# Optimization experiments

Hardware: AMD Instinct MI355X
Metric: run time of the kernel (lower is better)

Reference implementation:

```python
import jax, jax.numpy as jnp
import numpy as np

KEY_DIM = 512
VAL_DIM = 512
BATCH = 32768
MEMORY_MAX_NORM = 5.0
TTT_LR_SCALE = 0.005
EPS = 1e-8


def setup_inputs() -> dict:
    key = jax.random.key(0)
    k1, k2, k3, k4, k5 = jax.random.split(key, 5)
    k = jax.random.normal(k1, (BATCH, KEY_DIM), dtype=jnp.float32)
    v = jax.random.normal(k2, (BATCH, VAL_DIM), dtype=jnp.float32)
    # memory weight init: normal(std=0.01)
    mem_w = jax.random.normal(k3, (VAL_DIM, KEY_DIM), dtype=jnp.float32) * 0.01
    # gate_proj: init is zeros/0.5; use small random weight + 0.5 bias for a
    # non-degenerate but realistic post-warmup state
    gate_w = jax.random.normal(k4, (3, KEY_DIM + VAL_DIM), dtype=jnp.float32) * 0.01
    gate_b = jnp.full((3,), 0.5, dtype=jnp.float32)
    momentum_S = jax.random.normal(k5, (VAL_DIM, KEY_DIM), dtype=jnp.float32) * 0.01
    return {"k": k, "v": v, "mem_w": mem_w, "gate_w": gate_w,
            "gate_b": gate_b, "momentum_S": momentum_S}


def _norm_clip(x, max_norm):
    n = jnp.linalg.norm(x)
    return jnp.where(n > max_norm, x * (max_norm / (n + EPS)), x)


def reference(k, v, mem_w, gate_w, gate_b, momentum_S):
    # retrieve: M(k) = k @ W^T ; loss = MSE(pred, v)
    retrieved = k @ mem_w.T                      # [B, val_dim]
    diff = retrieved - v
    loss = jnp.mean(diff * diff)

    # gates from batch-mean key/value
    kv_agg = jnp.concatenate([k.mean(0), v.mean(0)], axis=-1)  # [key+val]
    gates = jax.nn.sigmoid(kv_agg @ gate_w.T + gate_b)         # [3]
    alpha, eta, theta = gates[0], gates[1], gates[2]

    # analytic grad of MSE wrt W: 2/(B*val_dim) * (pred - v)^T @ k
    B, vd = diff.shape
    grad = (2.0 / (B * vd)) * (diff.T @ k)       # [val_dim, key_dim]
    grad_c = jnp.clip(grad, -1.0, 1.0)

    new_momentum = eta * momentum_S - TTT_LR_SCALE * theta * grad_c
    new_momentum = _norm_clip(new_momentum, MEMORY_MAX_NORM)

    new_weight = (1.0 - alpha) * mem_w + new_momentum
    new_weight = _norm_clip(new_weight, MEMORY_MAX_NORM)

    return retrieved, loss, new_weight, new_momentum, alpha, eta, theta
```

## Files before the change

kernel.cpp:

```cpp
#include <hip/hip_runtime.h>
#include <math.h>


typedef __bf16 bf16x8 __attribute__((ext_vector_type(8)));
typedef float f32x4 __attribute__((ext_vector_type(4)));
typedef float float4_t __attribute__((ext_vector_type(4)));
typedef unsigned short ushort4_t __attribute__((ext_vector_type(4)));
typedef unsigned short ushort8_t __attribute__((ext_vector_type(8)));

#define OUT_LOSS   16777216
#define OUT_W      16777217
#define OUT_MOM    17039361
#define OUT_ALPHA  17301505

#define OFF_GRAD   0u
#define OFF_CKP    1048576u
#define OFF_CVP    2097152u
#define OFF_LOSSP  2621440u
#define OFF_COLK   2622464u
#define OFF_COLV   2624512u
#define OFF_SCAL   2626560u
#define OFF_K16    2626624u
#define OFF_W16    36181056u
#define OFF_DIFF   36705344u
#define OFF_MRAW   OFF_K16
#define OFF_WRAW   (OFF_K16 + 1048576u)

__device__ __forceinline__ unsigned short f2bf(float f) {
  union { float f; unsigned int u; } c; c.f = f;
  unsigned int u = c.u;
  u += 0x7fffu + ((u >> 16) & 1u);
  return (unsigned short)(u >> 16);
}

__device__ __forceinline__ void gload_lds16(const unsigned short* g, unsigned short* l) {
  __builtin_amdgcn_global_load_lds(
      (const __attribute__((address_space(1))) unsigned int*)g,
      (__attribute__((address_space(3))) unsigned int*)l, 16, 0, 0);
}

__global__ __launch_bounds__(256) void k1_convert(
    const float* __restrict__ Kp, const float* __restrict__ Wp,
    unsigned short* __restrict__ k16, unsigned short* __restrict__ w16,
    float* __restrict__ colk_part)
{
  __shared__ float cp[512];
  const int t = threadIdx.x;
  const int cg = t & 127;
  const int g = t >> 7;
  const int b = blockIdx.x;
  if (b < 512) {
    const int r0 = b << 6;
    float p0 = 0.f, p1 = 0.f, p2 = 0.f, p3 = 0.f;
#pragma unroll 4
    for (int rr = g; rr < 64; rr += 2) {
      const size_t off = (size_t)(r0 + rr) * 512 + (cg << 2);
      const float4_t v = *reinterpret_cast<const float4_t*>(&Kp[off]);
      ushort4_t h;
      h.x = f2bf(v.x); h.y = f2bf(v.y); h.z = f2bf(v.z); h.w = f2bf(v.w);
      *reinterpret_cast<ushort4_t*>(&k16[off]) = h;
      p0 += v.x; p1 += v.y; p2 += v.z; p3 += v.w;
    }
    if (g == 1) {
      cp[(cg << 2) + 0] = p0; cp[(cg << 2) + 1] = p1;
      cp[(cg << 2) + 2] = p2; cp[(cg << 2) + 3] = p3;
    }
    __syncthreads();
    if (g == 0) {
      colk_part[(size_t)b * 512 + (cg << 2) + 0] = p0 + cp[(cg << 2) + 0];
      colk_part[(size_t)b * 512 + (cg << 2) + 1] = p1 + cp[(cg << 2) + 1];
      colk_part[(size_t)b * 512 + (cg << 2) + 2] = p2 + cp[(cg << 2) + 2];
      colk_part[(size_t)b * 512 + (cg << 2) + 3] = p3 + cp[(cg << 2) + 3];
    }
  } else {
    const int r0 = (b - 512) << 5;
#pragma unroll 4
    for (int rr = g; rr < 32; rr += 2) {
      const size_t off = (size_t)(r0 + rr) * 512 + (cg << 2);
      const float4_t v = *reinterpret_cast<const float4_t*>(&Wp[off]);
      ushort4_t h;
      h.x = f2bf(v.x); h.y = f2bf(v.y); h.z = f2bf(v.z); h.w = f2bf(v.w);
      *reinterpret_cast<ushort4_t*>(&w16[off]) = h;
    }
  }
}

__global__ __launch_bounds__(256) void k2_gemm(
    const unsigned short* __restrict__ k16, const unsigned short* __restrict__ w16,
    const float* __restrict__ Vp, float* __restrict__ outp,
    unsigned short* __restrict__ diff16,
    float* __restrict__ colv_part, float* __restrict__ loss_part)
{
  __shared__ __align__(16) unsigned short As[8192];
  __shared__ __align__(16) unsigned short Bs[8192];
  __shared__ float redc[256];
  __shared__ float redl[4];

  const int t = threadIdx.x, lane = t & 63, wv = t >> 6;
  const int tile = (blockIdx.x & 7) * 128 + (blockIdx.x >> 3);
  const int rt = tile >> 2, vt = tile & 3;
  const int row0 = rt << 7, vd0 = vt << 7;

  f32x4 acc[4][4];
#pragma unroll
  for (int m = 0; m < 4; ++m)
#pragma unroll
    for (int n = 0; n < 4; ++n)
      acc[m][n] = (f32x4){0.f, 0.f, 0.f, 0.f};

  const int srow = (wv << 3) + (lane >> 3);
  const int scol = (lane & 7) << 3;
  const unsigned short* pA = k16 + (size_t)(row0 + srow) * 512 + scol;
  const unsigned short* pB = w16 + (size_t)(vd0 + srow) * 512 + scol;
  unsigned short* lA = &As[wv << 9];
  unsigned short* lB = &Bs[wv << 9];

  const int fr = lane & 15, fq = lane >> 4;
  const int wr = (wv >> 1) << 6, wc = (wv & 1) << 6;

  for (int kk0 = 0; kk0 < 512; kk0 += 64) {
#pragma unroll
    for (int i = 0; i < 4; ++i) {
      gload_lds16(pA + (i << 14) + kk0, lA + (i << 11));
      gload_lds16(pB + (i << 14) + kk0, lB + (i << 11));
    }
    __syncthreads();
#pragma unroll
    for (int kk = 0; kk < 64; kk += 32) {
      const int co = kk + (fq << 3);
      bf16x8 af[4], bfv[4];
#pragma unroll
      for (int m = 0; m < 4; ++m)
        af[m] = *reinterpret_cast<const bf16x8*>(&As[((wr + (m << 4) + fr) << 6) + co]);
#pragma unroll
      for (int n = 0; n < 4; ++n)
        bfv[n] = *reinterpret_cast<const bf16x8*>(&Bs[((wc + (n << 4) + fr) << 6) + co]);
#pragma unroll
      for (int m = 0; m < 4; ++m)
#pragma unroll
        for (int n = 0; n < 4; ++n)
          acc[m][n] = __builtin_amdgcn_mfma_f32_16x16x32_bf16(af[m], bfv[n], acc[m][n], 0, 0, 0);
    }
    __syncthreads();
  }

  float lsum = 0.f;
  float vcs[4] = {0.f, 0.f, 0.f, 0.f};
#pragma unroll
  for (int m = 0; m < 4; ++m) {
#pragma unroll
    for (int n = 0; n < 4; ++n) {
#pragma unroll
      for (int i = 0; i < 4; ++i) {
        const int gr = row0 + wr + (m << 4) + (fq << 2) + i;
        const int gc = vd0 + wc + (n << 4) + fr;
        const size_t oi = (size_t)gr * 512 + gc;
        const float rv = acc[m][n][i];
        outp[oi] = rv;
        const float vv = Vp[oi];
        const float d = rv - vv;
        lsum += d * d;
        vcs[n] += vv;
        diff16[oi] = f2bf(d);
      }
    }
  }
#pragma unroll
  for (int o = 32; o; o >>= 1) lsum += __shfl_xor(lsum, o);
  if (lane == 0) redl[wv] = lsum;
#pragma unroll
  for (int n = 0; n < 4; ++n) {
    vcs[n] += __shfl_xor(vcs[n], 16);
    vcs[n] += __shfl_xor(vcs[n], 32);
  }
  if (fq == 0) {
#pragma unroll
    for (int n = 0; n < 4; ++n)
      redc[(wv << 6) + (n << 4) + fr] = vcs[n];
  }
  __syncthreads();
  if (t < 128) {
    const int side = t >> 6, lc = t & 63;
    colv_part[(size_t)rt * 512 + vd0 + t] =
        redc[side * 64 + lc] + redc[(side + 2) * 64 + lc];
  }
  if (t == 0)
    atomicAdd(&loss_part[rt], redl[0] + redl[1] + redl[2] + redl[3]);
}

__global__ __launch_bounds__(256) void k3_grad(
    const unsigned short* __restrict__ diff16,
    const unsigned short* __restrict__ k16,
    float* __restrict__ grad)
{
  __shared__ __align__(16) unsigned short At[2][128][40];
  __shared__ __align__(16) unsigned short Bt[2][128][40];
  const int t = threadIdx.x;
  const int lane = t & 63;
  const int wv = t >> 6;
  const int b = blockIdx.x;
  const int x = b & 7;
  const int q = b >> 3;
  const int tile = q & 15;
  const int kc = ((q >> 4) << 3) | x;
  const int vd0 = (tile & 3) << 7;
  const int kd0 = (tile >> 2) << 7;
  const size_t r0 = (size_t)kc << 10;

  f32x4 acc[4][4];
#pragma unroll
  for (int m = 0; m < 4; ++m)
#pragma unroll
    for (int n = 0; n < 4; ++n)
      acc[m][n] = (f32x4){0.f, 0.f, 0.f, 0.f};

  const int dr = t >> 3;
  const int c0 = (t & 7) << 4;
  const int wr = (wv >> 1) << 6;
  const int wc = (wv & 1) << 6;
  const int fr = lane & 15;
  const int fq = lane >> 4;

  int cur = 0;
  for (int rr = 0; rr < 1024; rr += 32) {
    const size_t rowoff = (r0 + rr + dr) << 9;
    const ushort8_t a0 = *reinterpret_cast<const ushort8_t*>(&diff16[rowoff + vd0 + c0]);
    const ushort8_t a1 = *reinterpret_cast<const ushort8_t*>(&diff16[rowoff + vd0 + c0 + 8]);
    const ushort8_t b0 = *reinterpret_cast<const ushort8_t*>(&k16[rowoff + kd0 + c0]);
    const ushort8_t b1 = *reinterpret_cast<const ushort8_t*>(&k16[rowoff + kd0 + c0 + 8]);
    const int swz = ((c0 >> 4) & 3) << 3;
#pragma unroll
    for (int j = 0; j < 8; ++j) {
      const int drs = dr ^ swz;
      At[cur][c0 + j][drs] = a0[j];
      At[cur][c0 + 8 + j][drs] = a1[j];
      Bt[cur][c0 + j][drs] = b0[j];
      Bt[cur][c0 + 8 + j][drs] = b1[j];
    }
    __syncthreads();
    bf16x8 af[4], bfv[4];
#pragma unroll
    for (int m = 0; m < 4; ++m) {
      const int rA = wr + (m << 4) + fr;
      af[m] = *reinterpret_cast<const bf16x8*>(&At[cur][rA][(fq ^ ((rA >> 4) & 3)) << 3]);
    }
#pragma unroll
    for (int n = 0; n < 4; ++n) {
      const int rB = wc + (n << 4) + fr;
      bfv[n] = *reinterpret_cast<const bf16x8*>(&Bt[cur][rB][(fq ^ ((rB >> 4) & 3)) << 3]);
    }
#pragma unroll
    for (int m = 0; m < 4; ++m)
#pragma unroll
      for (int n = 0; n < 4; ++n)
        acc[m][n] = __builtin_amdgcn_mfma_f32_16x16x32_bf16(af[m], bfv[n], acc[m][n], 0, 0, 0);
    cur ^= 1;
  }
#pragma unroll
  for (int m = 0; m < 4; ++m)
#pragma unroll
    for (int n = 0; n < 4; ++n)
#pragma unroll
      for (int i = 0; i < 4; ++i)
        atomicAdd(&grad[(size_t)(vd0 + wr + (m << 4) + (fq << 2) + i) * 512
                        + kd0 + wc + (n << 4) + fr], acc[m][n][i]);
}

__global__ __launch_bounds__(256) void c1a_redcols(
    const float* __restrict__ ckp, const float* __restrict__ cvp,
    float* __restrict__ colk, float* __restrict__ colv)
{
  __shared__ float red[8][32];
  const int t = threadIdx.x, b = blockIdx.x;
  const int mtx = b >> 4;
  const int c = ((b & 15) << 5) + (t & 31);
  const int pg = t >> 5;
  const float* src = mtx ? cvp : ckp;
  const int P = mtx ? 256 : 512;
  float s = 0.f;
  for (int p = pg; p < P; p += 8) s += src[(size_t)p * 512 + c];
  red[pg][t & 31] = s;
  __syncthreads();
  if (pg == 0) {
    float tot = 0.f;
#pragma unroll
    for (int j = 0; j < 8; ++j) tot += red[j][t & 31];
    (mtx ? colv : colk)[c] = tot;
  }
}

__global__ __launch_bounds__(256) void c1b_gates(
    const float* __restrict__ gw, const float* __restrict__ gb,
    const float* __restrict__ colk, const float* __restrict__ colv,
    const float* __restrict__ lossp, float* __restrict__ scal,
    float* __restrict__ outp)
{
  __shared__ float red3[3][4];
  __shared__ float redl[4];
  const int t = threadIdx.x, lane = t & 63, wvi = t >> 6;
  float p[3] = {0.f, 0.f, 0.f};
  for (int j = t; j < 1024; j += 256) {
    const float kv = (j < 512 ? colk[j] : colv[j - 512]) * (1.0f / 32768.0f);
    p[0] += kv * gw[j];
    p[1] += kv * gw[1024 + j];
    p[2] += kv * gw[2048 + j];
  }
  float ls = lossp[t];
#pragma unroll
  for (int o = 32; o; o >>= 1) {
    ls += __shfl_xor(ls, o);
#pragma unroll
    for (int g = 0; g < 3; ++g) p[g] += __shfl_xor(p[g], o);
  }
  if (lane == 0) {
    red3[0][wvi] = p[0]; red3[1][wvi] = p[1]; red3[2][wvi] = p[2];
    redl[wvi] = ls;
  }
  __syncthreads();
  if (t == 0) {
    const float s0 = red3[0][0] + red3[0][1] + red3[0][2] + red3[0][3] + gb[0];
    const float s1 = red3[1][0] + red3[1][1] + red3[1][2] + red3[1][3] + gb[1];
    const float s2 = red3[2][0] + red3[2][1] + red3[2][2] + red3[2][3] + gb[2];
    const float alpha = 1.0f / (1.0f + expf(-s0));
    const float eta   = 1.0f / (1.0f + expf(-s1));
    const float theta = 1.0f / (1.0f + expf(-s2));
    scal[3] = alpha; scal[4] = eta; scal[5] = theta;
    outp[OUT_LOSS] = (redl[0] + redl[1] + redl[2] + redl[3]) * (1.0f / 16777216.0f);
    outp[OUT_ALPHA]     = alpha;
    outp[OUT_ALPHA + 1] = eta;
    outp[OUT_ALPHA + 2] = theta;
  }
}

__device__ __forceinline__ void block_atomic_sumsq(float sq, float* target) {
  __shared__ float red[4];
#pragma unroll
  for (int o = 32; o; o >>= 1) sq += __shfl_xor(sq, o);
  if ((threadIdx.x & 63) == 0) red[threadIdx.x >> 6] = sq;
  __syncthreads();
  if (threadIdx.x == 0) atomicAdd(target, red[0] + red[1] + red[2] + red[3]);
}

__global__ __launch_bounds__(256) void c2_mom(
    const float* __restrict__ grad, const float* __restrict__ S,
    float* scal, float* __restrict__ m_raw)
{
  const float eta = scal[4];
  const float cth = 0.005f * scal[5];
  const int i = ((blockIdx.x << 8) + threadIdx.x) << 2;
  const float4_t g = *reinterpret_cast<const float4_t*>(&grad[i]);
  const float4_t s = *reinterpret_cast<const float4_t*>(&S[i]);
  float4_t m; float sq = 0.f;
#pragma unroll
  for (int j = 0; j < 4; ++j) {
    float gj = g[j] * (2.0f / 16777216.0f);
    gj = fminf(1.0f, fmaxf(-1.0f, gj));
    m[j] = eta * s[j] - cth * gj;
    sq += m[j] * m[j];
  }
  *reinterpret_cast<float4_t*>(&m_raw[i]) = m;
  block_atomic_sumsq(sq, &scal[1]);
}

__global__ __launch_bounds__(256) void c3_wt(
    const float* __restrict__ m_raw, const float* __restrict__ memw,
    float* scal, float* __restrict__ w_raw, float* __restrict__ outp)
{
  const float nm = sqrtf(scal[1]);
  const float sm = nm > 5.0f ? 5.0f / (nm + 1e-8f) : 1.0f;
  const float oma = 1.0f - scal[3];
  const int i = ((blockIdx.x << 8) + threadIdx.x) << 2;
  const float4_t mr = *reinterpret_cast<const float4_t*>(&m_raw[i]);
  const float4_t wi = *reinterpret_cast<const float4_t*>(&memw[i]);
  float4_t w; float sq = 0.f;
#pragma unroll
  for (int j = 0; j < 4; ++j) {
    const float m = mr[j] * sm;
    outp[OUT_MOM + i + j] = m;
    w[j] = oma * wi[j] + m;
    sq += w[j] * w[j];
  }
  *reinterpret_cast<float4_t*>(&w_raw[i]) = w;
  block_atomic_sumsq(sq, &scal[2]);
}

__global__ __launch_bounds__(256) void c4_wt(
    const float* __restrict__ w_raw, const float* __restrict__ scal,
    float* __restrict__ outp)
{
  const float nw = sqrtf(scal[2]);
  const float sw = nw > 5.0f ? 5.0f / (nw + 1e-8f) : 1.0f;
  const int i = ((blockIdx.x << 8) + threadIdx.x) << 2;
  const float4_t w = *reinterpret_cast<const float4_t*>(&w_raw[i]);
#pragma unroll
  for (int j = 0; j < 4; ++j)
    outp[OUT_W + i + j] = w[j] * sw;
}

extern "C" void kernel_launch(void* const* d_in, const int* in_sizes, int n_in,
                              void* d_out, int out_size, void* d_ws, size_t ws_size,
                              hipStream_t stream)
{
  const float* Kp = (const float*)d_in[0];
  const float* Vp = (const float*)d_in[1];
  const float* Wp = (const float*)d_in[2];
  const float* GW = (const float*)d_in[3];
  const float* GB = (const float*)d_in[4];
  const float* Sp = (const float*)d_in[5];
  float* outp = (float*)d_out;
  char* ws = (char*)d_ws;

  float* grad            = (float*)(ws + OFF_GRAD);
  float* colk_part       = (float*)(ws + OFF_CKP);
  float* colv_part       = (float*)(ws + OFF_CVP);
  float* loss_part       = (float*)(ws + OFF_LOSSP);
  float* colk            = (float*)(ws + OFF_COLK);
  float* colv            = (float*)(ws + OFF_COLV);
  float* scal            = (float*)(ws + OFF_SCAL);
  unsigned short* k16    = (unsigned short*)(ws + OFF_K16);
  unsigned short* w16    = (unsigned short*)(ws + OFF_W16);
  unsigned short* diff16 = (unsigned short*)(ws + OFF_DIFF);
  float* m_raw           = (float*)(ws + OFF_MRAW);
  float* w_raw           = (float*)(ws + OFF_WRAW);

  hipMemsetAsync(ws + OFF_GRAD, 0, 1048576, stream);
  hipMemsetAsync(ws + OFF_LOSSP, 0, OFF_SCAL + 64 - OFF_LOSSP, stream);

  k1_convert<<<528, 256, 0, stream>>>(Kp, Wp, k16, w16, colk_part);
  k2_gemm<<<1024, 256, 0, stream>>>(k16, w16, Vp, outp, diff16, colv_part, loss_part);
  k3_grad<<<512, 256, 0, stream>>>(diff16, k16, grad);
  c1a_redcols<<<32, 256, 0, stream>>>(colk_part, colv_part, colk, colv);
  c1b_gates<<<1, 256, 0, stream>>>(GW, GB, colk, colv, loss_part, scal, outp);
  c2_mom<<<256, 256, 0, stream>>>(grad, Sp, scal, m_raw);
  c3_wt<<<256, 256, 0, stream>>>(m_raw, Wp, scal, w_raw, outp);
  c4_wt<<<256, 256, 0, stream>>>(w_raw, scal, outp);
}
```

Before: 183.8 us.

## Fuse fp32-to-bf16 conversion into GEMM and move column sums into grad kernel

Drops the separate conversion kernel. The GEMM now loads fp32 K and W directly, converts them to bf16 into padded LDS, and writes the bf16 K copy once per row tile. Column sums of K move into the gradient kernel, atomics into grad are spread across four slabs, and the two-stage reduction kernel is merged into the gates kernel. This removes a full pass over K and two launches, but the GEMM loses its async global-to-LDS loads, reads W in fp32 redundantly, and the single-block gates kernel now does a larger serial reduction.

```diff
diff --git a/kernel.cpp b/kernel.cpp
--- a/kernel.cpp
+++ b/kernel.cpp
@@ -14,85 +14,34 @@
 #define OUT_ALPHA  17301505
 
 #define OFF_GRAD   0u
-#define OFF_CKP    1048576u
-#define OFF_CVP    2097152u
-#define OFF_LOSSP  2621440u
-#define OFF_COLK   2622464u
-#define OFF_COLV   2624512u
-#define OFF_SCAL   2626560u
-#define OFF_K16    2626624u
-#define OFF_W16    36181056u
-#define OFF_DIFF   36705344u
+#define OFF_CKP    4194304u
+#define OFF_CVP    4259840u
+#define OFF_LOSSP  4784128u
+#define OFF_SCAL   4788224u
+#define OFF_K16    4788288u
+#define OFF_DIFF   38342720u
 #define OFF_MRAW   OFF_K16
 #define OFF_WRAW   (OFF_K16 + 1048576u)
 
-__device__ __forceinline__ unsigned short f2bf(float f) {
-  union { float f; unsigned int u; } c; c.f = f;
-  unsigned int u = c.u;
-  u += 0x7fffu + ((u >> 16) & 1u);
-  return (unsigned short)(u >> 16);
-}
-
-__device__ __forceinline__ void gload_lds16(const unsigned short* g, unsigned short* l) {
-  __builtin_amdgcn_global_load_lds(
-      (const __attribute__((address_space(1))) unsigned int*)g,
-      (__attribute__((address_space(3))) unsigned int*)l, 16, 0, 0);
-}
-
-__global__ __launch_bounds__(256) void k1_convert(
+__device__ __forceinline__ ushort4_t cvt4(float4_t v) {
+  union { __bf16 b; unsigned short u; } c0, c1, c2, c3;
+  c0.b = (__bf16)v.x; c1.b = (__bf16)v.y; c2.b = (__bf16)v.z; c3.b = (__bf16)v.w;
+  ushort4_t h; h.x = c0.u; h.y = c1.u; h.z = c2.u; h.w = c3.u;
+  return h;
+}
+
+__device__ __forceinline__ float bf2f(unsigned short u) {
+  return __uint_as_float(((unsigned int)u) << 16);
+}
+
+__global__ __launch_bounds__(256) void k2_gemm(
     const float* __restrict__ Kp, const float* __restrict__ Wp,
-    unsigned short* __restrict__ k16, unsigned short* __restrict__ w16,
-    float* __restrict__ colk_part)
-{
-  __shared__ float cp[512];
-  const int t = threadIdx.x;
-  const int cg = t & 127;
-  const int g = t >> 7;
-  const int b = blockIdx.x;
-  if (b < 512) {
-    const int r0 = b << 6;
-    float p0 = 0.f, p1 = 0.f, p2 = 0.f, p3 = 0.f;
-#pragma unroll 4
-    for (int rr = g; rr < 64; rr += 2) {
-      const size_t off = (size_t)(r0 + rr) * 512 + (cg << 2);
-      const float4_t v = *reinterpret_cast<const float4_t*>(&Kp[off]);
-      ushort4_t h;
-      h.x = f2bf(v.x); h.y = f2bf(v.y); h.z = f2bf(v.z); h.w = f2bf(v.w);
-      *reinterpret_cast<ushort4_t*>(&k16[off]) = h;
-      p0 += v.x; p1 += v.y; p2 += v.z; p3 += v.w;
-    }
-    if (g == 1) {
-      cp[(cg << 2) + 0] = p0; cp[(cg << 2) + 1] = p1;
-      cp[(cg << 2) + 2] = p2; cp[(cg << 2) + 3] = p3;
-    }
-    __syncthreads();
-    if (g == 0) {
-      colk_part[(size_t)b * 512 + (cg << 2) + 0] = p0 + cp[(cg << 2) + 0];
-      colk_part[(size_t)b * 512 + (cg << 2) + 1] = p1 + cp[(cg << 2) + 1];
-      colk_part[(size_t)b * 512 + (cg << 2) + 2] = p2 + cp[(cg << 2) + 2];
-      colk_part[(size_t)b * 512 + (cg << 2) + 3] = p3 + cp[(cg << 2) + 3];
-    }
-  } else {
-    const int r0 = (b - 512) << 5;
-#pragma unroll 4
-    for (int rr = g; rr < 32; rr += 2) {
-      const size_t off = (size_t)(r0 + rr) * 512 + (cg << 2);
-      const float4_t v = *reinterpret_cast<const float4_t*>(&Wp[off]);
-      ushort4_t h;
-      h.x = f2bf(v.x); h.y = f2bf(v.y); h.z = f2bf(v.z); h.w = f2bf(v.w);
-      *reinterpret_cast<ushort4_t*>(&w16[off]) = h;
-    }
-  }
-}
-
-__global__ __launch_bounds__(256) void k2_gemm(
-    const unsigned short* __restrict__ k16, const unsigned short* __restrict__ w16,
     const float* __restrict__ Vp, float* __restrict__ outp,
-    unsigned short* __restrict__ diff16,
+    unsigned short* __restrict__ k16, unsigned short* __restrict__ diff16,
     float* __restrict__ colv_part, float* __restrict__ loss_part)
 {
-  __shared__ __align__(16) unsigned short As[8192];
-  __shared__ __align__(16) unsigned short Bs[8192];
+  __shared__ __align__(16) unsigned short As[128 * 72];
+  __shared__ __align__(16) unsigned short Bs[128 * 72];
   __shared__ float redc[256];
   __shared__ float redl[4];
 
@@ -108,21 +57,24 @@
     for (int n = 0; n < 4; ++n)
       acc[m][n] = (f32x4){0.f, 0.f, 0.f, 0.f};
 
-  const int srow = (wv << 3) + (lane >> 3);
-  const int scol = (lane & 7) << 3;
-  const unsigned short* pA = k16 + (size_t)(row0 + srow) * 512 + scol;
-  const unsigned short* pB = w16 + (size_t)(vd0 + srow) * 512 + scol;
-  unsigned short* lA = &As[wv << 9];
-  unsigned short* lB = &Bs[wv << 9];
-
+  const int srow = t >> 4;
+  const int scol = (t & 15) << 2;
   const int fr = lane & 15, fq = lane >> 4;
   const int wr = (wv >> 1) << 6, wc = (wv & 1) << 6;
 
   for (int kk0 = 0; kk0 < 512; kk0 += 64) {
 #pragma unroll
-    for (int i = 0; i < 4; ++i) {
-      gload_lds16(pA + (i << 14) + kk0, lA + (i << 11));
-      gload_lds16(pB + (i << 14) + kk0, lB + (i << 11));
+    for (int p = 0; p < 8; ++p) {
+      const int r = (p << 4) + srow;
+      const size_t ga = (size_t)(row0 + r) * 512 + kk0 + scol;
+      const float4_t av = *reinterpret_cast<const float4_t*>(&Kp[ga]);
+      const ushort4_t ah = cvt4(av);
+      *reinterpret_cast<ushort4_t*>(&As[r * 72 + scol]) = ah;
+      if ((p >> 1) == vt)
+        *reinterpret_cast<ushort4_t*>(&k16[ga]) = ah;
+      const size_t gb = (size_t)(vd0 + r) * 512 + kk0 + scol;
+      const float4_t bv = *reinterpret_cast<const float4_t*>(&Wp[gb]);
+      *reinterpret_cast<ushort4_t*>(&Bs[r * 72 + scol]) = cvt4(bv);
     }
     __syncthreads();
 #pragma unroll
@@ -131,10 +83,10 @@
       bf16x8 af[4], bfv[4];
 #pragma unroll
       for (int m = 0; m < 4; ++m)
-        af[m] = *reinterpret_cast<const bf16x8*>(&As[((wr + (m << 4) + fr) << 6) + co]);
+        af[m] = *reinterpret_cast<const bf16x8*>(&As[(wr + (m << 4) + fr) * 72 + co]);
 #pragma unroll
       for (int n = 0; n < 4; ++n)
-        bfv[n] = *reinterpret_cast<const bf16x8*>(&Bs[((wc + (n << 4) + fr) << 6) + co]);
+        bfv[n] = *reinterpret_cast<const bf16x8*>(&Bs[(wc + (n << 4) + fr) * 72 + co]);
 #pragma unroll
       for (int m = 0; m < 4; ++m)
 #pragma unroll
@@ -161,7 +113,8 @@
         const float d = rv - vv;
         lsum += d * d;
         vcs[n] += vv;
-        diff16[oi] = f2bf(d);
+        union { __bf16 b; unsigned short u; } cd; cd.b = (__bf16)d;
+        diff16[oi] = cd.u;
       }
     }
   }
@@ -185,13 +138,13 @@
         redc[side * 64 + lc] + redc[(side + 2) * 64 + lc];
   }
   if (t == 0)
-    atomicAdd(&loss_part[rt], redl[0] + redl[1] + redl[2] + redl[3]);
+    loss_part[tile] = redl[0] + redl[1] + redl[2] + redl[3];
 }
 
 __global__ __launch_bounds__(256) void k3_grad(
     const unsigned short* __restrict__ diff16,
     const unsigned short* __restrict__ k16,
-    float* __restrict__ grad)
+    float* __restrict__ grad_part, float* __restrict__ colk_part)
 {
   __shared__ __align__(16) unsigned short At[2][128][40];
   __shared__ __align__(16) unsigned short Bt[2][128][40];
@@ -214,6 +167,10 @@
     for (int n = 0; n < 4; ++n)
       acc[m][n] = (f32x4){0.f, 0.f, 0.f, 0.f};
 
+  float ck[16];
+#pragma unroll
+  for (int j = 0; j < 16; ++j) ck[j] = 0.f;
+
   const int dr = t >> 3;
   const int c0 = (t & 7) << 4;
   const int wr = (wv >> 1) << 6;
@@ -228,6 +185,10 @@
     const ushort8_t a1 = *reinterpret_cast<const ushort8_t*>(&diff16[rowoff + vd0 + c0 + 8]);
     const ushort8_t b0 = *reinterpret_cast<const ushort8_t*>(&k16[rowoff + kd0 + c0]);
     const ushort8_t b1 = *reinterpret_cast<const ushort8_t*>(&k16[rowoff + kd0 + c0 + 8]);
+    if (vd0 == 0) {
+#pragma unroll
+      for (int j = 0; j < 8; ++j) { ck[j] += bf2f(b0[j]); ck[8 + j] += bf2f(b1[j]); }
+    }
     const int swz = ((c0 >> 4) & 3) << 3;
 #pragma unroll
     for (int j = 0; j < 8; ++j) {
@@ -256,66 +217,76 @@
         acc[m][n] = __builtin_amdgcn_mfma_f32_16x16x32_bf16(af[m], bfv[n], acc[m][n], 0, 0, 0);
     cur ^= 1;
   }
+
+  float* gslab = grad_part + (size_t)(kc & 3) * 262144;
 #pragma unroll
   for (int m = 0; m < 4; ++m)
 #pragma unroll
     for (int n = 0; n < 4; ++n)
 #pragma unroll
       for (int i = 0; i < 4; ++i)
-        atomicAdd(&grad[(size_t)(vd0 + wr + (m << 4) + (fq << 2) + i) * 512
-                        + kd0 + wc + (n << 4) + fr], acc[m][n][i]);
-}
-
-__global__ __launch_bounds__(256) void c1a_redcols(
+        atomicAdd(&gslab[(size_t)(vd0 + wr + (m << 4) + (fq << 2) + i) * 512
+                         + kd0 + wc + (n << 4) + fr], acc[m][n][i]);
+
+  if (vd0 == 0) {
+#pragma unroll
+    for (int j = 0; j < 16; ++j) {
+      ck[j] += __shfl_xor(ck[j], 8);
+      ck[j] += __shfl_xor(ck[j], 16);
+      ck[j] += __shfl_xor(ck[j], 32);
+    }
+    __syncthreads();
+    float* cred = (float*)&At[0][0][0];
+    if (lane < 8) {
+#pragma unroll
+      for (int j = 0; j < 16; ++j) cred[(wv << 7) + (lane << 4) + j] = ck[j];
+    }
+    __syncthreads();
+    if (t < 128) {
+      colk_part[(size_t)kc * 512 + kd0 + t] =
+          cred[t] + cred[128 + t] + cred[256 + t] + cred[384 + t];
+    }
+  }
+}
+
+__global__ __launch_bounds__(256) void c1_gates(
+    const float* __restrict__ gw, const float* __restrict__ gb,
     const float* __restrict__ ckp, const float* __restrict__ cvp,
-    float* __restrict__ colk, float* __restrict__ colv)
-{
-  __shared__ float red[8][32];
-  const int t = threadIdx.x, b = blockIdx.x;
-  const int mtx = b >> 4;
-  const int c = ((b & 15) << 5) + (t & 31);
-  const int pg = t >> 5;
-  const float* src = mtx ? cvp : ckp;
-  const int P = mtx ? 256 : 512;
-  float s = 0.f;
-  for (int p = pg; p < P; p += 8) s += src[(size_t)p * 512 + c];
-  red[pg][t & 31] = s;
-  __syncthreads();
-  if (pg == 0) {
-    float tot = 0.f;
-#pragma unroll
-    for (int j = 0; j < 8; ++j) tot += red[j][t & 31];
-    (mtx ? colv : colk)[c] = tot;
-  }
-}
-
-__global__ __launch_bounds__(256) void c1b_gates(
-    const float* __restrict__ gw, const float* __restrict__ gb,
-    const float* __restrict__ colk, const float* __restrict__ colv,
     const float* __restrict__ lossp, float* __restrict__ scal,
     float* __restrict__ outp)
 {
+  __shared__ float ck[512], cv[512];
   __shared__ float red3[3][4];
   __shared__ float redl[4];
   const int t = threadIdx.x, lane = t & 63, wvi = t >> 6;
-  float p[3] = {0.f, 0.f, 0.f};
+
+  for (int c = t; c < 512; c += 256) {
+    float s = 0.f;
+    for (int p = 0; p < 32; ++p) s += ckp[(size_t)p * 512 + c];
+    ck[c] = s;
+    float s2 = 0.f;
+    for (int p = 0; p < 256; ++p) s2 += cvp[(size_t)p * 512 + c];
+    cv[c] = s2;
+  }
+  float ls = lossp[t] + lossp[256 + t] + lossp[512 + t] + lossp[768 + t];
+#pragma unroll
+  for (int o = 32; o; o >>= 1) ls += __shfl_xor(ls, o);
+  if (lane == 0) redl[wvi] = ls;
+  __syncthreads();
+
+  float p3[3] = {0.f, 0.f, 0.f};
   for (int j = t; j < 1024; j += 256) {
-    const float kv = (j < 512 ? colk[j] : colv[j - 512]) * (1.0f / 32768.0f);
-    p[0] += kv * gw[j];
-    p[1] += kv * gw[1024 + j];
-    p[2] += kv * gw[2048 + j];
-  }
-  float ls = lossp[t];
+    const float kv = (j < 512 ? ck[j] : cv[j - 512]) * (1.0f / 32768.0f);
+    p3[0] += kv * gw[j];
+    p3[1] += kv * gw[1024 + j];
+    p3[2] += kv * gw[2048 + j];
+  }
 #pragma unroll
   for (int o = 32; o; o >>= 1) {
-    ls += __shfl_xor(ls, o);
-#pragma unroll
-    for (int g = 0; g < 3; ++g) p[g] += __shfl_xor(p[g], o);
-  }
-  if (lane == 0) {
-    red3[0][wvi] = p[0]; red3[1][wvi] = p[1]; red3[2][wvi] = p[2];
-    redl[wvi] = ls;
-  }
+#pragma unroll
+    for (int g = 0; g < 3; ++g) p3[g] += __shfl_xor(p3[g], o);
+  }
+  if (lane == 0) { red3[0][wvi] = p3[0]; red3[1][wvi] = p3[1]; red3[2][wvi] = p3[2]; }
   __syncthreads();
   if (t == 0) {
     const float s0 = red3[0][0] + red3[0][1] + red3[0][2] + red3[0][3] + gb[0];
@@ -324,6 +295,7 @@
     const float alpha = 1.0f / (1.0f + expf(-s0));
     const float eta   = 1.0f / (1.0f + expf(-s1));
     const float theta = 1.0f / (1.0f + expf(-s2));
+    scal[1] = 0.f; scal[2] = 0.f;
     scal[3] = alpha; scal[4] = eta; scal[5] = theta;
     outp[OUT_LOSS] = (redl[0] + redl[1] + redl[2] + redl[3]) * (1.0f / 16777216.0f);
     outp[OUT_ALPHA]     = alpha;
@@ -342,18 +314,21 @@
 }
 
 __global__ __launch_bounds__(256) void c2_mom(
-    const float* __restrict__ grad, const float* __restrict__ S,
+    const float* __restrict__ grad_part, const float* __restrict__ S,
     float* scal, float* __restrict__ m_raw)
 {
   const float eta = scal[4];
   const float cth = 0.005f * scal[5];
   const int i = ((blockIdx.x << 8) + threadIdx.x) << 2;
-  const float4_t g = *reinterpret_cast<const float4_t*>(&grad[i]);
+  float4_t g = *reinterpret_cast<const float4_t*>(&grad_part[i]);
+  const float4_t g1 = *reinterpret_cast<const float4_t*>(&grad_part[262144 + i]);
+  const float4_t g2 = *reinterpret_cast<const float4_t*>(&grad_part[524288 + i]);
+  const float4_t g3 = *reinterpret_cast<const float4_t*>(&grad_part[786432 + i]);
   const float4_t s = *reinterpret_cast<const float4_t*>(&S[i]);
   float4_t m; float sq = 0.f;
 #pragma unroll
   for (int j = 0; j < 4; ++j) {
-    float gj = g[j] * (2.0f / 16777216.0f);
+    float gj = (g[j] + g1[j] + g2[j] + g3[j]) * (2.0f / 16777216.0f);
     gj = fminf(1.0f, fmaxf(-1.0f, gj));
     m[j] = eta * s[j] - cth * gj;
     sq += m[j] * m[j];
@@ -410,28 +385,22 @@
   float* outp = (float*)d_out;
   char* ws = (char*)d_ws;
 
-  float* grad            = (float*)(ws + OFF_GRAD);
+  float* grad_part       = (float*)(ws + OFF_GRAD);
   float* colk_part       = (float*)(ws + OFF_CKP);
   float* colv_part       = (float*)(ws + OFF_CVP);
   float* loss_part       = (float*)(ws + OFF_LOSSP);
-  float* colk            = (float*)(ws + OFF_COLK);
-  float* colv            = (float*)(ws + OFF_COLV);
   float* scal            = (float*)(ws + OFF_SCAL);
   unsigned short* k16    = (unsigned short*)(ws + OFF_K16);
-  unsigned short* w16    = (unsigned short*)(ws + OFF_W16);
   unsigned short* diff16 = (unsigned short*)(ws + OFF_DIFF);
   float* m_raw           = (float*)(ws + OFF_MRAW);
   float* w_raw           = (float*)(ws + OFF_WRAW);
 
-  hipMemsetAsync(ws + OFF_GRAD, 0, 1048576, stream);
-  hipMemsetAsync(ws + OFF_LOSSP, 0, OFF_SCAL + 64 - OFF_LOSSP, stream);
-
-  k1_convert<<<528, 256, 0, stream>>>(Kp, Wp, k16, w16, colk_part);
-  k2_gemm<<<1024, 256, 0, stream>>>(k16, w16, Vp, outp, diff16, colv_part, loss_part);
-  k3_grad<<<512, 256, 0, stream>>>(diff16, k16, grad);
-  c1a_redcols<<<32, 256, 0, stream>>>(colk_part, colv_part, colk, colv);
-  c1b_gates<<<1, 256, 0, stream>>>(GW, GB, colk, colv, loss_part, scal, outp);
-  c2_mom<<<256, 256, 0, stream>>>(grad, Sp, scal, m_raw);
+  hipMemsetAsync(ws + OFF_GRAD, 0, 4194304, stream);
+
+  k2_gemm<<<1024, 256, 0, stream>>>(Kp, Wp, Vp, outp, k16, diff16, colv_part, loss_part);
+  k3_grad<<<512, 256, 0, stream>>>(diff16, k16, grad_part, colk_part);
+  c1_gates<<<1, 256, 0, stream>>>(GW, GB, colk_part, colv_part, loss_part, scal, outp);
+  c2_mom<<<256, 256, 0, stream>>>(grad_part, Sp, scal, m_raw);
   c3_wt<<<256, 256, 0, stream>>>(m_raw, Wp, scal, w_raw, outp);
   c4_wt<<<256, 256, 0, stream>>>(w_raw, scal, outp);
 }
```

Measured after the change: 219.4 us. 1.19x slower.

## Shrink GEMM tiles to 128x64, halve convert blocks, drop loss atomics and memset

Applied to the files above, without the earlier changes.

The forward GEMM now uses 128x64 output tiles over 2048 blocks instead of 128x128 over 1024, so fewer accumulators are live and more blocks are resident. Per-tile loss partials are written directly rather than atomically added, and the gates kernel sums all 2048 of them, which removes the second memset. The K conversion uses 128-row blocks, cutting the colk partials from 512 to 256, and float-to-bf16 uses native casts. The smaller tiles reload the K operand twice as often, raising global and LDS traffic.

```diff
diff --git a/kernel.cpp b/kernel.cpp
--- a/kernel.cpp
+++ b/kernel.cpp
@@ -15,22 +15,22 @@
 
 #define OFF_GRAD   0u
 #define OFF_CKP    1048576u
-#define OFF_CVP    2097152u
-#define OFF_LOSSP  2621440u
-#define OFF_COLK   2622464u
-#define OFF_COLV   2624512u
-#define OFF_SCAL   2626560u
-#define OFF_K16    2626624u
-#define OFF_W16    36181056u
-#define OFF_DIFF   36705344u
+#define OFF_CVP    1572864u
+#define OFF_LOSSP  2097152u
+#define OFF_COLK   2105344u
+#define OFF_COLV   2107392u
+#define OFF_SCAL   2109440u
+#define OFF_W16    2109504u
+#define OFF_K16    2633792u
+#define OFF_DIFF   36188224u
 #define OFF_MRAW   OFF_K16
 #define OFF_WRAW   (OFF_K16 + 1048576u)
 
-__device__ __forceinline__ unsigned short f2bf(float f) {
-  union { float f; unsigned int u; } c; c.f = f;
-  unsigned int u = c.u;
-  u += 0x7fffu + ((u >> 16) & 1u);
-  return (unsigned short)(u >> 16);
+__device__ __forceinline__ ushort4_t cvt4(float4_t v) {
+  union { __bf16 b; unsigned short u; } c0, c1, c2, c3;
+  c0.b = (__bf16)v.x; c1.b = (__bf16)v.y; c2.b = (__bf16)v.z; c3.b = (__bf16)v.w;
+  ushort4_t h; h.x = c0.u; h.y = c1.u; h.z = c2.u; h.w = c3.u;
+  return h;
 }
 
 __device__ __forceinline__ void gload_lds16(const unsigned short* g, unsigned short* l) {
@@ -49,16 +49,14 @@
   const int cg = t & 127;
   const int g = t >> 7;
   const int b = blockIdx.x;
-  if (b < 512) {
-    const int r0 = b << 6;
+  if (b < 256) {
+    const int r0 = b << 7;
     float p0 = 0.f, p1 = 0.f, p2 = 0.f, p3 = 0.f;
 #pragma unroll 4
-    for (int rr = g; rr < 64; rr += 2) {
+    for (int rr = g; rr < 128; rr += 2) {
       const size_t off = (size_t)(r0 + rr) * 512 + (cg << 2);
       const float4_t v = *reinterpret_cast<const float4_t*>(&Kp[off]);
-      ushort4_t h;
-      h.x = f2bf(v.x); h.y = f2bf(v.y); h.z = f2bf(v.z); h.w = f2bf(v.w);
-      *reinterpret_cast<ushort4_t*>(&k16[off]) = h;
+      *reinterpret_cast<ushort4_t*>(&k16[off]) = cvt4(v);
       p0 += v.x; p1 += v.y; p2 += v.z; p3 += v.w;
     }
     if (g == 1) {
@@ -73,14 +71,12 @@
       colk_part[(size_t)b * 512 + (cg << 2) + 3] = p3 + cp[(cg << 2) + 3];
     }
   } else {
-    const int r0 = (b - 512) << 5;
+    const int r0 = (b - 256) << 5;
 #pragma unroll 4
     for (int rr = g; rr < 32; rr += 2) {
       const size_t off = (size_t)(r0 + rr) * 512 + (cg << 2);
       const float4_t v = *reinterpret_cast<const float4_t*>(&Wp[off]);
-      ushort4_t h;
-      h.x = f2bf(v.x); h.y = f2bf(v.y); h.z = f2bf(v.z); h.w = f2bf(v.w);
-      *reinterpret_cast<ushort4_t*>(&w16[off]) = h;
+      *reinterpret_cast<ushort4_t*>(&w16[off]) = cvt4(v);
     }
   }
 }
@@ -92,20 +88,20 @@
     float* __restrict__ colv_part, float* __restrict__ loss_part)
 {
   __shared__ __align__(16) unsigned short As[8192];
-  __shared__ __align__(16) unsigned short Bs[8192];
-  __shared__ float redc[256];
+  __shared__ __align__(16) unsigned short Bs[4096];
+  __shared__ float redc[128];
   __shared__ float redl[4];
 
   const int t = threadIdx.x, lane = t & 63, wv = t >> 6;
-  const int tile = (blockIdx.x & 7) * 128 + (blockIdx.x >> 3);
-  const int rt = tile >> 2, vt = tile & 3;
-  const int row0 = rt << 7, vd0 = vt << 7;
-
-  f32x4 acc[4][4];
+  const int tile = (blockIdx.x & 7) * 256 + (blockIdx.x >> 3);
+  const int rt = tile >> 3, vt = tile & 7;
+  const int row0 = rt << 7, vd0 = vt << 6;
+
+  f32x4 acc[4][2];
 #pragma unroll
   for (int m = 0; m < 4; ++m)
 #pragma unroll
-    for (int n = 0; n < 4; ++n)
+    for (int n = 0; n < 2; ++n)
       acc[m][n] = (f32x4){0.f, 0.f, 0.f, 0.f};
 
   const int srow = (wv << 3) + (lane >> 3);
@@ -116,52 +112,54 @@
   unsigned short* lB = &Bs[wv << 9];
 
   const int fr = lane & 15, fq = lane >> 4;
-  const int wr = (wv >> 1) << 6, wc = (wv & 1) << 6;
+  const int wr = (wv >> 1) << 6, wc = (wv & 1) << 5;
 
   for (int kk0 = 0; kk0 < 512; kk0 += 64) {
 #pragma unroll
-    for (int i = 0; i < 4; ++i) {
+    for (int i = 0; i < 4; ++i)
       gload_lds16(pA + (i << 14) + kk0, lA + (i << 11));
+#pragma unroll
+    for (int i = 0; i < 2; ++i)
       gload_lds16(pB + (i << 14) + kk0, lB + (i << 11));
-    }
     __syncthreads();
 #pragma unroll
     for (int kk = 0; kk < 64; kk += 32) {
       const int co = kk + (fq << 3);
-      bf16x8 af[4], bfv[4];
+      bf16x8 af[4], bfv[2];
 #pragma unroll
       for (int m = 0; m < 4; ++m)
         af[m] = *reinterpret_cast<const bf16x8*>(&As[((wr + (m << 4) + fr) << 6) + co]);
 #pragma unroll
-      for (int n = 0; n < 4; ++n)
+      for (int n = 0; n < 2; ++n)
         bfv[n] = *reinterpret_cast<const bf16x8*>(&Bs[((wc + (n << 4) + fr) << 6) + co]);
 #pragma unroll
       for (int m = 0; m < 4; ++m)
 #pragma unroll
-        for (int n = 0; n < 4; ++n)
+        for (int n = 0; n < 2; ++n)
           acc[m][n] = __builtin_amdgcn_mfma_f32_16x16x32_bf16(af[m], bfv[n], acc[m][n], 0, 0, 0);
     }
     __syncthreads();
   }
 
   float lsum = 0.f;
-  float vcs[4] = {0.f, 0.f, 0.f, 0.f};
+  float vcs[2] = {0.f, 0.f};
 #pragma unroll
   for (int m = 0; m < 4; ++m) {
 #pragma unroll
-    for (int n = 0; n < 4; ++n) {
+    for (int n = 0; n < 2; ++n) {
 #pragma unroll
       for (int i = 0; i < 4; ++i) {
-        const int gr = row0 + wr + (m << 4) + (fq << 2) + i;
-        const int gc = vd0 + wc + (n << 4) + fr;
-        const size_t oi = (size_t)gr * 512 + gc;
+        const int rl = wr + (m << 4) + (fq << 2) + i;
+        const int cl = wc + (n << 4) + fr;
+        const size_t oi = (size_t)(row0 + rl) * 512 + vd0 + cl;
         const float rv = acc[m][n][i];
         outp[oi] = rv;
         const float vv = Vp[oi];
         const float d = rv - vv;
         lsum += d * d;
         vcs[n] += vv;
-        diff16[oi] = f2bf(d);
+        union { __bf16 b; unsigned short u; } cd; cd.b = (__bf16)d;
+        diff16[oi] = cd.u;
       }
     }
   }
@@ -169,23 +167,23 @@
   for (int o = 32; o; o >>= 1) lsum += __shfl_xor(lsum, o);
   if (lane == 0) redl[wv] = lsum;
 #pragma unroll
-  for (int n = 0; n < 4; ++n) {
+  for (int n = 0; n < 2; ++n) {
     vcs[n] += __shfl_xor(vcs[n], 16);
     vcs[n] += __shfl_xor(vcs[n], 32);
   }
   if (fq == 0) {
 #pragma unroll
-    for (int n = 0; n < 4; ++n)
-      redc[(wv << 6) + (n << 4) + fr] = vcs[n];
+    for (int n = 0; n < 2; ++n)
+      redc[(wv << 5) + (n << 4) + fr] = vcs[n];
   }
   __syncthreads();
-  if (t < 128) {
-    const int side = t >> 6, lc = t & 63;
+  if (t < 64) {
+    const int h = t >> 5, lc = t & 31;
     colv_part[(size_t)rt * 512 + vd0 + t] =
-        redc[side * 64 + lc] + redc[(side + 2) * 64 + lc];
+        redc[(h << 5) + lc] + redc[((h + 2) << 5) + lc];
   }
   if (t == 0)
-    atomicAdd(&loss_part[rt], redl[0] + redl[1] + redl[2] + redl[3]);
+    loss_part[tile] = redl[0] + redl[1] + redl[2] + redl[3];
 }
 
 __global__ __launch_bounds__(256) void k3_grad(
@@ -276,9 +274,8 @@
   const int c = ((b & 15) << 5) + (t & 31);
   const int pg = t >> 5;
   const float* src = mtx ? cvp : ckp;
-  const int P = mtx ? 256 : 512;
   float s = 0.f;
-  for (int p = pg; p < P; p += 8) s += src[(size_t)p * 512 + c];
+  for (int p = pg; p < 256; p += 8) s += src[(size_t)p * 512 + c];
   red[pg][t & 31] = s;
   __syncthreads();
   if (pg == 0) {
@@ -298,22 +295,24 @@
   __shared__ float red3[3][4];
   __shared__ float redl[4];
   const int t = threadIdx.x, lane = t & 63, wvi = t >> 6;
-  float p[3] = {0.f, 0.f, 0.f};
+  float p3[3] = {0.f, 0.f, 0.f};
   for (int j = t; j < 1024; j += 256) {
     const float kv = (j < 512 ? colk[j] : colv[j - 512]) * (1.0f / 32768.0f);
-    p[0] += kv * gw[j];
-    p[1] += kv * gw[1024 + j];
-    p[2] += kv * gw[2048 + j];
-  }
-  float ls = lossp[t];
+    p3[0] += kv * gw[j];
+    p3[1] += kv * gw[1024 + j];
+    p3[2] += kv * gw[2048 + j];
+  }
+  float ls = 0.f;
+#pragma unroll
+  for (int q = 0; q < 8; ++q) ls += lossp[t + (q << 8)];
 #pragma unroll
   for (int o = 32; o; o >>= 1) {
     ls += __shfl_xor(ls, o);
 #pragma unroll
-    for (int g = 0; g < 3; ++g) p[g] += __shfl_xor(p[g], o);
+    for (int g = 0; g < 3; ++g) p3[g] += __shfl_xor(p3[g], o);
   }
   if (lane == 0) {
-    red3[0][wvi] = p[0]; red3[1][wvi] = p[1]; red3[2][wvi] = p[2];
+    red3[0][wvi] = p3[0]; red3[1][wvi] = p3[1]; red3[2][wvi] = p3[2];
     redl[wvi] = ls;
   }
   __syncthreads();
@@ -324,6 +323,7 @@
     const float alpha = 1.0f / (1.0f + expf(-s0));
     const float eta   = 1.0f / (1.0f + expf(-s1));
     const float theta = 1.0f / (1.0f + expf(-s2));
+    scal[1] = 0.f; scal[2] = 0.f;
     scal[3] = alpha; scal[4] = eta; scal[5] = theta;
     outp[OUT_LOSS] = (redl[0] + redl[1] + redl[2] + redl[3]) * (1.0f / 16777216.0f);
     outp[OUT_ALPHA]     = alpha;
@@ -417,17 +417,16 @@
   float* colk            = (float*)(ws + OFF_COLK);
   float* colv            = (float*)(ws + OFF_COLV);
   float* scal            = (float*)(ws + OFF_SCAL);
+  unsigned short* w16    = (unsigned short*)(ws + OFF_W16);
   unsigned short* k16    = (unsigned short*)(ws + OFF_K16);
-  unsigned short* w16    = (unsigned short*)(ws + OFF_W16);
   unsigned short* diff16 = (unsigned short*)(ws + OFF_DIFF);
   float* m_raw           = (float*)(ws + OFF_MRAW);
   float* w_raw           = (float*)(ws + OFF_WRAW);
 
   hipMemsetAsync(ws + OFF_GRAD, 0, 1048576, stream);
-  hipMemsetAsync(ws + OFF_LOSSP, 0, OFF_SCAL + 64 - OFF_LOSSP, stream);
-
-  k1_convert<<<528, 256, 0, stream>>>(Kp, Wp, k16, w16, colk_part);
-  k2_gemm<<<1024, 256, 0, stream>>>(k16, w16, Vp, outp, diff16, colv_part, loss_part);
+
+  k1_convert<<<272, 256, 0, stream>>>(Kp, Wp, k16, w16, colk_part);
+  k2_gemm<<<2048, 256, 0, stream>>>(k16, w16, Vp, outp, diff16, colv_part, loss_part);
   k3_grad<<<512, 256, 0, stream>>>(diff16, k16, grad);
   c1a_redcols<<<32, 256, 0, stream>>>(colk_part, colv_part, colk, colv);
   c1b_gates<<<1, 256, 0, stream>>>(GW, GB, colk, colv, loss_part, scal, outp);
```

After: 173.6 us. 1.06x faster.
